# Kernel tuning notes

Hardware: AMD Instinct MI355X
Metric: run time of the kernel (lower is better)

## Reference

```python
import jax, jax.numpy as jnp
import numpy as np

N_NODES = 50000
N_EDGES = 800000
N_GRAPHS = 64
HID = 128
FEAT = 64
OUT = 32
N_LAYERS = 3
DECAY = 0.9
THRESH = 0.1


def setup_inputs() -> dict:
    key = jax.random.key(0)
    ks = jax.random.split(key, 24)
    s = 0.05
    inp = {
        "x": jax.random.normal(ks[0], (N_NODES, FEAT), jnp.float32),
        "edge_attr": jax.random.normal(ks[1], (N_EDGES, 1), jnp.float32),
        "initial_importance": jax.random.uniform(ks[2], (N_NODES, 1), jnp.float32),
        "imp_proj_W": jax.random.normal(ks[3], (1, HID), jnp.float32) * s,
        "imp_proj_b": jnp.zeros((HID,), jnp.float32),
        "init_W": jax.random.normal(ks[4], (FEAT + HID, HID), jnp.float32) * s,
        "init_b": jnp.zeros((HID,), jnp.float32),
        "msg_W": jax.random.normal(ks[5], (N_LAYERS, HID, HID), jnp.float32) * s,
        "msg_b": jnp.zeros((N_LAYERS, HID), jnp.float32),
        "upd_W": jax.random.normal(ks[6], (N_LAYERS, 2 * HID, HID), jnp.float32) * s,
        "upd_b": jnp.zeros((N_LAYERS, HID), jnp.float32),
        "gate_W": jax.random.normal(ks[7], (N_LAYERS, HID + 1, HID), jnp.float32) * s,
        "gate_b": jnp.zeros((N_LAYERS, HID), jnp.float32),
        "prop_W": jax.random.normal(ks[8], (N_LAYERS, HID, 1), jnp.float32) * s,
        "prop_b": jnp.zeros((N_LAYERS, 1), jnp.float32),
        "norm_w": jnp.ones((N_LAYERS, HID), jnp.float32),
        "norm_b": jnp.zeros((N_LAYERS, HID), jnp.float32),
        "norm_a": jnp.ones((N_LAYERS, HID), jnp.float32),
        "final_W": jax.random.normal(ks[9], (HID, OUT), jnp.float32) * s,
        "final_b": jnp.zeros((OUT,), jnp.float32),
        "edge_index": jax.random.randint(ks[10], (2, N_EDGES), 0, N_NODES, jnp.int32),
        # evenly spread sorted graph ids -> every graph non-empty
        "batch": (jnp.arange(N_NODES, dtype=jnp.int32) * N_GRAPHS) // N_NODES,
    }
    return inp


def _normalize_importance(imp, batch):
    # per-graph min/max normalization, fused segment reductions
    mn = jax.ops.segment_min(imp, batch, num_segments=N_GRAPHS)[batch]
    mx = jax.ops.segment_max(imp, batch, num_segments=N_GRAPHS)[batch]
    return (imp - mn) / (mx - mn + 1e-8)


def _graph_norm(x, batch, counts, w, b, a):
    # PyG GraphNorm: y = w * (x - a*mean) / sqrt(var(x - a*mean) + eps) + b
    mean = jax.ops.segment_sum(x, batch, num_segments=N_GRAPHS) / counts
    out = x - a * mean[batch]
    var = jax.ops.segment_sum(out * out, batch, num_segments=N_GRAPHS) / counts
    std = jnp.sqrt(var + 1e-5)
    return w * out / std[batch] + b


def _forward(x, edge_attr, initial_importance, imp_proj_W, imp_proj_b, init_W,
             init_b, msg_W, msg_b, upd_W, upd_b, gate_W, gate_b, prop_W, prop_b,
             norm_w, norm_b, norm_a, final_W, final_b, edge_index, batch):
    src, dst = edge_index[0], edge_index[1]
    counts = jax.ops.segment_sum(jnp.ones((N_NODES, 1), x.dtype), batch,
                                 num_segments=N_GRAPHS)  # [G,1]

    imp0 = initial_importance[:, 0]                       # [N]
    importance = _normalize_importance(imp0, batch)       # [N]
    imp_emb = importance[:, None] @ imp_proj_W + imp_proj_b  # [N,H]
    h = jnp.concatenate([x, imp_emb], axis=-1) @ init_W + init_b  # [N,H]

    for l in range(N_LAYERS):
        # MPNN: gather -> linear -> scatter-add -> update
        msg = h[src] @ msg_W[l] + msg_b[l]                # [E,H]
        aggr = jax.ops.segment_sum(msg, dst, num_segments=N_NODES)  # [N,H]
        conv = jnp.concatenate([h, aggr], axis=-1) @ upd_W[l] + upd_b[l]
        # importance gating
        gate_in = jnp.concatenate([conv, importance[:, None]], axis=-1)
        gate = jax.nn.sigmoid(gate_in @ gate_W[l] + gate_b[l])
        out = gate * conv + (1.0 - gate) * h
        prop = out @ prop_W[l] + prop_b[l]                # [N,1]
        # norm + relu (dropout p=0 in eval)
        h = jax.nn.relu(_graph_norm(out, batch, counts, norm_w[l], norm_b[l], norm_a[l]))
        # importance update
        imp = DECAY * importance + (1.0 - DECAY) * prop[:, 0]
        imp = _normalize_importance(imp, batch)
        imp = jnp.where(imp < THRESH, 0.0, imp)
        importance = _normalize_importance(imp, batch)

    h = h @ final_W + final_b                             # [N,OUT]
    logits = jax.ops.segment_sum(h, batch, num_segments=N_GRAPHS) / counts  # [G,OUT]
    final_importance = _normalize_importance(imp0 + importance, batch)
    return logits, final_importance[:, None]


def reference(x, edge_attr, initial_importance, imp_proj_W, imp_proj_b, init_W,
              init_b, msg_W, msg_b, upd_W, upd_b, gate_W, gate_b, prop_W, prop_b,
              norm_w, norm_b, norm_a, final_W, final_b, edge_index, batch):
    return _forward(x, edge_attr, initial_importance, imp_proj_W, imp_proj_b,
                    init_W, init_b, msg_W, msg_b, upd_W, upd_b, gate_W, gate_b,
                    prop_W, prop_b, norm_w, norm_b, norm_a, final_W, final_b,
                    edge_index, batch)
```

## Files before the change

### kernel.cpp

```cpp
#include <hip/hip_runtime.h>
#include <cstdint>

#define NN 50000
#define NE 800000
#define NG 64
#define HD 128
#define FT 64
#define NLAYERS 3
#define MB 32
#define NBLK 1563

__global__ void k_gbounds(const int* __restrict__ batch, int* __restrict__ gstart){
    int i = blockIdx.x*blockDim.x + threadIdx.x;
    if (i >= NN) return;
    int g = batch[i];
    if (i == 0){ for (int q = 0; q <= g; ++q) gstart[q] = 0; }
    else { int gp = batch[i-1]; for (int q = gp+1; q <= g; ++q) gstart[q] = i; }
    if (i == NN-1){ for (int q = g+1; q <= NG; ++q) gstart[q] = NN; }
}

__device__ __forceinline__ void block_minmax(float lmn, float lmx, float* red,
                                             float& omn, float& omx){
    #pragma unroll
    for (int off = 32; off > 0; off >>= 1){
        lmn = fminf(lmn, __shfl_xor(lmn, off));
        lmx = fmaxf(lmx, __shfl_xor(lmx, off));
    }
    int wave = threadIdx.x >> 6;
    if ((threadIdx.x & 63) == 0){ red[wave] = lmn; red[4+wave] = lmx; }
    __syncthreads();
    omn = fminf(fminf(red[0], red[1]), fminf(red[2], red[3]));
    omx = fmaxf(fmaxf(red[4], red[5]), fmaxf(red[6], red[7]));
    __syncthreads();
}

__global__ __launch_bounds__(256) void k_norm_graph(
    const float* __restrict__ va, const int* __restrict__ gstart,
    float* __restrict__ out)
{
    __shared__ float sv[1024];
    __shared__ float red[8];
    int g = blockIdx.x;
    int s = gstart[g], n = gstart[g+1] - s;
    int tid = threadIdx.x;
    float lmn = 3.4e38f, lmx = -3.4e38f;
    for (int i = tid; i < n; i += 256){
        float v = va[s+i];
        sv[i] = v;
        lmn = fminf(lmn, v); lmx = fmaxf(lmx, v);
    }
    float lo, hi;
    block_minmax(lmn, lmx, red, lo, hi);
    float inv = 1.f/(hi - lo + 1e-8f);
    for (int i = tid; i < n; i += 256) out[s+i] = (sv[i] - lo)*inv;
}

__global__ void k_fold_init(const float* __restrict__ pW, const float* __restrict__ pb,
                            const float* __restrict__ iW, const float* __restrict__ ib,
                            float* __restrict__ W0, float* __restrict__ b0){
    int j = threadIdx.x;
    for (int k = 0; k < FT; ++k) W0[k*HD + j] = iW[k*HD + j];
    float w2 = 0.f, b2 = 0.f;
    for (int k = 0; k < HD; ++k){
        float w = iW[(FT + k)*HD + j];
        w2 += pW[k]*w;
        b2 += pb[k]*w;
    }
    W0[FT*HD + j] = w2;
    b0[j] = ib[j] + b2;
}

__global__ void k_fold_layer(const float* __restrict__ msgW, const float* __restrict__ updW,
                             const float* __restrict__ msgb,
                             float* __restrict__ WfA, float* __restrict__ bcvA){
    int l = blockIdx.y;
    const float* mW  = msgW + (size_t)l*HD*HD;
    const float* uW  = updW + (size_t)l*2*HD*HD;
    const float* mb  = msgb + (size_t)l*HD;
    float* Wf  = WfA  + (size_t)l*2*HD*HD;
    float* bcv = bcvA + (size_t)l*HD;
    int j = threadIdx.x;
    int r = blockIdx.x;
    if (r < HD){
        Wf[(size_t)r*HD + j] = uW[(size_t)r*HD + j];
    } else if (r < 2*HD){
        int rr = r - HD;
        const float* uWbot = uW + (size_t)HD*HD;
        float acc = 0.f;
        for (int k = 0; k < HD; ++k)
            acc = fmaf(mW[(size_t)rr*HD + k], uWbot[(size_t)k*HD + j], acc);
        Wf[(size_t)r*HD + j] = acc;
    } else {
        const float* uWbot = uW + (size_t)HD*HD;
        float acc = 0.f;
        for (int k = 0; k < HD; ++k)
            acc = fmaf(mb[k], uWbot[(size_t)k*HD + j], acc);
        bcv[j] = acc;
    }
}

__global__ __launch_bounds__(256) void k_init(
    const float* __restrict__ x, const float* __restrict__ imp,
    const float* __restrict__ W0, const float* __restrict__ b0v,
    float* __restrict__ h)
{
    __shared__ float lds[MB][FT];
    __shared__ float scs[MB];
    int base = blockIdx.x*MB, tid = threadIdx.x;
    #pragma unroll
    for (int i = 0; i < 2; ++i){
        int fidx = i*256 + tid;
        int t = fidx >> 4, c = fidx & 15;
        float4 v = {0.f,0.f,0.f,0.f};
        if (base + t < NN) v = *(const float4*)&x[(size_t)(base+t)*FT + c*4];
        *(float4*)&lds[t][c*4] = v;
    }
    if (tid < MB) scs[tid] = (base+tid < NN) ? imp[base+tid] : 0.f;
    __syncthreads();

    const int cg = tid & 31, rg = tid >> 5;
    const int c0 = cg*4, r0 = rg*4;
    const float4 wl4 = *(const float4*)&W0[(size_t)FT*HD + c0];
    const float4 b4  = *(const float4*)&b0v[c0];
    float acc[4][4];
    #pragma unroll
    for (int r = 0; r < 4; ++r){
        float s = scs[r0+r];
        acc[r][0] = fmaf(s, wl4.x, b4.x); acc[r][1] = fmaf(s, wl4.y, b4.y);
        acc[r][2] = fmaf(s, wl4.z, b4.z); acc[r][3] = fmaf(s, wl4.w, b4.w);
    }
    #pragma unroll 4
    for (int k4 = 0; k4 < 16; ++k4){
        const float4 w0 = *(const float4*)&W0[(size_t)(k4*4+0)*HD + c0];
        const float4 w1 = *(const float4*)&W0[(size_t)(k4*4+1)*HD + c0];
        const float4 w2 = *(const float4*)&W0[(size_t)(k4*4+2)*HD + c0];
        const float4 w3 = *(const float4*)&W0[(size_t)(k4*4+3)*HD + c0];
        #pragma unroll
        for (int r = 0; r < 4; ++r){
            const float4 a = *(const float4*)&lds[r0+r][k4*4];
            acc[r][0]=fmaf(a.x,w0.x,fmaf(a.y,w1.x,fmaf(a.z,w2.x,fmaf(a.w,w3.x,acc[r][0]))));
            acc[r][1]=fmaf(a.x,w0.y,fmaf(a.y,w1.y,fmaf(a.z,w2.y,fmaf(a.w,w3.y,acc[r][1]))));
            acc[r][2]=fmaf(a.x,w0.z,fmaf(a.y,w1.z,fmaf(a.z,w2.z,fmaf(a.w,w3.z,acc[r][2]))));
            acc[r][3]=fmaf(a.x,w0.w,fmaf(a.y,w1.w,fmaf(a.z,w2.w,fmaf(a.w,w3.w,acc[r][3]))));
        }
    }
    #pragma unroll
    for (int r = 0; r < 4; ++r)
        if (base + r0 + r < NN)
            *(float4*)&h[(size_t)(base+r0+r)*HD + c0] =
                make_float4(acc[r][0], acc[r][1], acc[r][2], acc[r][3]);
}

#define FMA8(r, a, b, W0_,W1_,W2_,W3_,W4_,W5_,W6_,W7_, A) \
    A[r][0]=fmaf((b).x,W4_.x,fmaf((b).y,W5_.x,fmaf((b).z,W6_.x,fmaf((b).w,W7_.x, \
            fmaf((a).x,W0_.x,fmaf((a).y,W1_.x,fmaf((a).z,W2_.x,fmaf((a).w,W3_.x,A[r][0])))))))); \
    A[r][1]=fmaf((b).x,W4_.y,fmaf((b).y,W5_.y,fmaf((b).z,W6_.y,fmaf((b).w,W7_.y, \
            fmaf((a).x,W0_.y,fmaf((a).y,W1_.y,fmaf((a).z,W2_.y,fmaf((a).w,W3_.y,A[r][1])))))))); \
    A[r][2]=fmaf((b).x,W4_.z,fmaf((b).y,W5_.z,fmaf((b).z,W6_.z,fmaf((b).w,W7_.z, \
            fmaf((a).x,W0_.z,fmaf((a).y,W1_.z,fmaf((a).z,W2_.z,fmaf((a).w,W3_.z,A[r][2])))))))); \
    A[r][3]=fmaf((b).x,W4_.w,fmaf((b).y,W5_.w,fmaf((b).z,W6_.w,fmaf((b).w,W7_.w, \
            fmaf((a).x,W0_.w,fmaf((a).y,W1_.w,fmaf((a).z,W2_.w,fmaf((a).w,W3_.w,A[r][3]))))))));

__global__ __launch_bounds__(256, 4) void k_layer(
    const float* __restrict__ h, const float* __restrict__ aggr,
    const float* __restrict__ imp, const int* __restrict__ deg,
    const float* __restrict__ Wf, const float* __restrict__ bcv,
    const float* __restrict__ ub,
    const float* __restrict__ gW, const float* __restrict__ gb,
    const float* __restrict__ prW, const float* __restrict__ prb,
    float* __restrict__ outbuf, float* __restrict__ ta)
{
    __shared__ float lds[MB][256];
    __shared__ float scs[MB];
    __shared__ float dgs[MB];
    __shared__ float red[8][4];
    const int base = blockIdx.x*MB, tid = threadIdx.x;

    #pragma unroll
    for (int i = 0; i < 8; ++i){
        int fidx = i*256 + tid;
        int t = fidx >> 6, c = fidx & 63;
        float4 v = {0.f,0.f,0.f,0.f};
        if (base + t < NN){
            const float* srcp = (c < 32) ? &h[(size_t)(base+t)*HD + c*4]
                                         : &aggr[(size_t)(base+t)*HD + (c-32)*4];
            v = *(const float4*)srcp;
        }
        *(float4*)&lds[t][c*4] = v;
    }
    if (tid < MB) scs[tid] = (base+tid < NN) ? imp[base+tid] : 0.f;
    else if (tid < 2*MB){
        int t = tid - MB;
        dgs[t] = (base+t < NN) ? (float)deg[base+t] : 0.f;
    }
    __syncthreads();

    const int cg = tid & 31, rg = tid >> 5;
    const int c0 = cg*4, r0 = rg*4;

    const float4* wv = (const float4*)Wf;
    const float4 bc4 = *(const float4*)&bcv[c0];
    const float4 ub4 = *(const float4*)&ub[c0];
    float acc[4][4];
    #pragma unroll
    for (int r = 0; r < 4; ++r){
        float d = dgs[r0+r];
        acc[r][0] = fmaf(d, bc4.x, ub4.x); acc[r][1] = fmaf(d, bc4.y, ub4.y);
        acc[r][2] = fmaf(d, bc4.z, ub4.z); acc[r][3] = fmaf(d, bc4.w, ub4.w);
    }
    {
        const float4* p0 = wv + cg;
        float4 n0 = p0[0],   n1 = p0[32],  n2 = p0[64],  n3 = p0[96];
        float4 n4 = p0[128], n5 = p0[160], n6 = p0[192], n7 = p0[224];
        for (int kb = 0; kb < 256; kb += 8){
            const float4 w0=n0,w1=n1,w2=n2,w3=n3,w4=n4,w5=n5,w6=n6,w7=n7;
            if (kb + 8 < 256){
                const float4* np = wv + (size_t)(kb+8)*32 + cg;
                n0=np[0];   n1=np[32];  n2=np[64];  n3=np[96];
                n4=np[128]; n5=np[160]; n6=np[192]; n7=np[224];
            }
            #pragma unroll
            for (int r = 0; r < 4; ++r){
                const float4 a = *(const float4*)&lds[r0+r][kb];
                const float4 b = *(const float4*)&lds[r0+r][kb+4];
                FMA8(r, a, b, w0,w1,w2,w3,w4,w5,w6,w7, acc)
            }
        }
    }
    __syncthreads();
    #pragma unroll
    for (int r = 0; r < 4; ++r)
        *(float4*)&lds[r0+r][HD + c0] = make_float4(acc[r][0],acc[r][1],acc[r][2],acc[r][3]);
    __syncthreads();

    const float4* gv = (const float4*)gW;
    const float4 gwl = gv[(size_t)HD*32 + cg];
    const float4 gb4 = *(const float4*)&gb[c0];
    float z[4][4];
    #pragma unroll
    for (int r = 0; r < 4; ++r){
        float s = scs[r0+r];
        z[r][0] = fmaf(s, gwl.x, gb4.x); z[r][1] = fmaf(s, gwl.y, gb4.y);
        z[r][2] = fmaf(s, gwl.z, gb4.z); z[r][3] = fmaf(s, gwl.w, gb4.w);
    }
    {
        const float4* p0 = gv + cg;
        float4 n0 = p0[0],   n1 = p0[32],  n2 = p0[64],  n3 = p0[96];
        float4 n4 = p0[128], n5 = p0[160], n6 = p0[192], n7 = p0[224];
        for (int kb = 0; kb < 128; kb += 8){
            const float4 w0=n0,w1=n1,w2=n2,w3=n3,w4=n4,w5=n5,w6=n6,w7=n7;
            if (kb + 8 < 128){
                const float4* np = gv + (size_t)(kb+8)*32 + cg;
                n0=np[0];   n1=np[32];  n2=np[64];  n3=np[96];
                n4=np[128]; n5=np[160]; n6=np[192]; n7=np[224];
            }
            #pragma unroll
            for (int r = 0; r < 4; ++r){
                const float4 a = *(const float4*)&lds[r0+r][HD + kb];
                const float4 b = *(const float4*)&lds[r0+r][HD + kb+4];
                FMA8(r, a, b, w0,w1,w2,w3,w4,w5,w6,w7, z)
            }
        }
    }

    const float4 pr4 = *(const float4*)&prW[c0];
    float psum[4];
    #pragma unroll
    for (int r = 0; r < 4; ++r){
        const float4 hv = *(const float4*)&lds[r0+r][c0];
        float g0 = 1.f/(1.f + expf(-z[r][0]));
        float g1 = 1.f/(1.f + expf(-z[r][1]));
        float g2 = 1.f/(1.f + expf(-z[r][2]));
        float g3 = 1.f/(1.f + expf(-z[r][3]));
        float o0 = g0*acc[r][0] + (1.f-g0)*hv.x;
        float o1 = g1*acc[r][1] + (1.f-g1)*hv.y;
        float o2 = g2*acc[r][2] + (1.f-g2)*hv.z;
        float o3 = g3*acc[r][3] + (1.f-g3)*hv.w;
        if (base + r0 + r < NN)
            *(float4*)&outbuf[(size_t)(base+r0+r)*HD + c0] = make_float4(o0,o1,o2,o3);
        psum[r] = o0*pr4.x + o1*pr4.y + o2*pr4.z + o3*pr4.w;
    }
    #pragma unroll
    for (int r = 0; r < 4; ++r){
        float v = psum[r];
        #pragma unroll
        for (int off = 16; off > 0; off >>= 1) v += __shfl_xor(v, off);
        if (cg == 0) red[rg][r] = v;
    }
    __syncthreads();
    if (tid < MB && base + tid < NN)
        ta[base+tid] = 0.9f*scs[tid] + 0.1f*(red[tid>>2][tid&3] + prb[0]);
}

__global__ void k_deg(const int* __restrict__ dst, int* deg){
    int e = blockIdx.x*blockDim.x + threadIdx.x;
    if (e < NE) atomicAdd(&deg[dst[e]], 1);
}

__global__ __launch_bounds__(1024) void k_scan(const int* __restrict__ deg,
                                               int* __restrict__ rowstart){
    __shared__ int wtot[16];
    __shared__ int woff[16];
    __shared__ int carry;
    int tid = threadIdx.x, lane = tid & 63, wv = tid >> 6;
    if (tid == 0) carry = 0;
    __syncthreads();
    for (int base = 0; base < NN; base += 1024){
        int i = base + tid;
        int v = (i < NN) ? deg[i] : 0;
        int x = v;
        #pragma unroll
        for (int off = 1; off < 64; off <<= 1){
            int y = __shfl_up(x, off);
            if (lane >= off) x += y;
        }
        if (lane == 63) wtot[wv] = x;
        __syncthreads();
        if (tid == 0){
            int a = carry;
            for (int w2 = 0; w2 < 16; ++w2){ woff[w2] = a; a += wtot[w2]; }
            carry = a;
        }
        __syncthreads();
        if (i < NN) rowstart[i] = woff[wv] + x - v;
    }
    __syncthreads();
    if (tid == 0) rowstart[NN] = carry;
}

__global__ void k_copy_int(const int* __restrict__ a, int* __restrict__ b, int n){
    int i = blockIdx.x*blockDim.x + threadIdx.x;
    if (i < n) b[i] = a[i];
}

__global__ void k_fill(const int* __restrict__ src, const int* __restrict__ dst,
                       int* cursor, int* __restrict__ csr){
    int e = blockIdx.x*blockDim.x + threadIdx.x;
    if (e < NE){
        int d = dst[e];
        int p = atomicAdd(&cursor[d], 1);
        csr[p] = src[e];
    }
}

__global__ __launch_bounds__(256) void k_aggregate(
    const float* __restrict__ hm, const int* __restrict__ rowstart,
    const int* __restrict__ csr, float* __restrict__ aggr)
{
    int node = blockIdx.x*8 + (threadIdx.x >> 5);
    int lane = threadIdx.x & 31;
    float4 a0 = {0.f,0.f,0.f,0.f}, a1 = a0, a2 = a0, a3 = a0;
    float4 a4 = a0, a5 = a0, a6 = a0, a7 = a0;
    int e0 = rowstart[node], e1 = rowstart[node+1];
    int e = e0;
    for (; e + 7 < e1; e += 8){
        int s0 = csr[e],   s1 = csr[e+1], s2 = csr[e+2], s3 = csr[e+3];
        int s4 = csr[e+4], s5 = csr[e+5], s6 = csr[e+6], s7 = csr[e+7];
        const float4 v0 = *(const float4*)&hm[(size_t)s0*HD + lane*4];
        const float4 v1 = *(const float4*)&hm[(size_t)s1*HD + lane*4];
        const float4 v2 = *(const float4*)&hm[(size_t)s2*HD + lane*4];
        const float4 v3 = *(const float4*)&hm[(size_t)s3*HD + lane*4];
        const float4 v4 = *(const float4*)&hm[(size_t)s4*HD + lane*4];
        const float4 v5 = *(const float4*)&hm[(size_t)s5*HD + lane*4];
        const float4 v6 = *(const float4*)&hm[(size_t)s6*HD + lane*4];
        const float4 v7 = *(const float4*)&hm[(size_t)s7*HD + lane*4];
        a0.x += v0.x; a0.y += v0.y; a0.z += v0.z; a0.w += v0.w;
        a1.x += v1.x; a1.y += v1.y; a1.z += v1.z; a1.w += v1.w;
        a2.x += v2.x; a2.y += v2.y; a2.z += v2.z; a2.w += v2.w;
        a3.x += v3.x; a3.y += v3.y; a3.z += v3.z; a3.w += v3.w;
        a4.x += v4.x; a4.y += v4.y; a4.z += v4.z; a4.w += v4.w;
        a5.x += v5.x; a5.y += v5.y; a5.z += v5.z; a5.w += v5.w;
        a6.x += v6.x; a6.y += v6.y; a6.z += v6.z; a6.w += v6.w;
        a7.x += v7.x; a7.y += v7.y; a7.z += v7.z; a7.w += v7.w;
    }
    for (; e + 3 < e1; e += 4){
        int s0 = csr[e], s1 = csr[e+1], s2 = csr[e+2], s3 = csr[e+3];
        const float4 v0 = *(const float4*)&hm[(size_t)s0*HD + lane*4];
        const float4 v1 = *(const float4*)&hm[(size_t)s1*HD + lane*4];
        const float4 v2 = *(const float4*)&hm[(size_t)s2*HD + lane*4];
        const float4 v3 = *(const float4*)&hm[(size_t)s3*HD + lane*4];
        a0.x += v0.x; a0.y += v0.y; a0.z += v0.z; a0.w += v0.w;
        a1.x += v1.x; a1.y += v1.y; a1.z += v1.z; a1.w += v1.w;
        a2.x += v2.x; a2.y += v2.y; a2.z += v2.z; a2.w += v2.w;
        a3.x += v3.x; a3.y += v3.y; a3.z += v3.z; a3.w += v3.w;
    }
    for (; e < e1; ++e){
        int s0 = csr[e];
        const float4 v0 = *(const float4*)&hm[(size_t)s0*HD + lane*4];
        a0.x += v0.x; a0.y += v0.y; a0.z += v0.z; a0.w += v0.w;
    }
    a0.x += a1.x; a0.y += a1.y; a0.z += a1.z; a0.w += a1.w;
    a2.x += a3.x; a2.y += a3.y; a2.z += a3.z; a2.w += a3.w;
    a4.x += a5.x; a4.y += a5.y; a4.z += a5.z; a4.w += a5.w;
    a6.x += a7.x; a6.y += a7.y; a6.z += a7.z; a6.w += a7.w;
    a0.x += a2.x; a0.y += a2.y; a0.z += a2.z; a0.w += a2.w;
    a4.x += a6.x; a4.y += a6.y; a4.z += a6.z; a4.w += a6.w;
    a0.x += a4.x; a0.y += a4.y; a0.z += a4.z; a0.w += a4.w;
    *(float4*)&aggr[(size_t)node*HD + lane*4] = a0;
}

__global__ __launch_bounds__(256) void k_gnorm(
    const float* __restrict__ v, const int* __restrict__ gstart,
    const float* __restrict__ nw, const float* __restrict__ nb,
    const float* __restrict__ na, float* __restrict__ hout,
    const float* __restrict__ tsrc, float* __restrict__ tdst)
{
    int g = blockIdx.x;
    int part = blockIdx.y;
    int s = gstart[g], n = gstart[g+1] - s;
    int tid = threadIdx.x;

    if (part == 4){
        __shared__ float sv[1024];
        __shared__ float red[8];
        float lmn = 3.4e38f, lmx = -3.4e38f;
        for (int i = tid; i < n; i += 256){
            float val = tsrc[s+i]; sv[i] = val;
            lmn = fminf(lmn, val); lmx = fmaxf(lmx, val);
        }
        float lo, hi;
        block_minmax(lmn, lmx, red, lo, hi);
        float inv = 1.f/(hi - lo + 1e-8f);
        lmn = 3.4e38f; lmx = -3.4e38f;
        for (int i = tid; i < n; i += 256){
            float t2 = (sv[i] - lo)*inv;
            if (t2 < 0.1f) t2 = 0.f;
            sv[i] = t2;
            lmn = fminf(lmn, t2); lmx = fmaxf(lmx, t2);
        }
        float lo2, hi2;
        block_minmax(lmn, lmx, red, lo2, hi2);
        float inv2 = 1.f/(hi2 - lo2 + 1e-8f);
        for (int i = tid; i < n; i += 256) tdst[s+i] = (sv[i] - lo2)*inv2;
        return;
    }

    __shared__ float4 rs1[32][8];
    __shared__ float4 rs2[32][8];
    __shared__ float amv[32], scv[32], nbv[32];
    int rg = tid >> 3, c4l = tid & 7;
    size_t coff = (size_t)part*32 + c4l*4;
    float4 s1 = {0.f,0.f,0.f,0.f}, s2 = {0.f,0.f,0.f,0.f};
    for (int i = rg; i < n; i += 32){
        const float4 vv = *(const float4*)&v[(size_t)(s+i)*HD + coff];
        s1.x += vv.x; s1.y += vv.y; s1.z += vv.z; s1.w += vv.w;
        s2.x += vv.x*vv.x; s2.y += vv.y*vv.y; s2.z += vv.z*vv.z; s2.w += vv.w*vv.w;
    }
    rs1[rg][c4l] = s1; rs2[rg][c4l] = s2;
    __syncthreads();
    if (tid < 8){
        float4 t1 = {0.f,0.f,0.f,0.f}, t2 = {0.f,0.f,0.f,0.f};
        for (int r = 0; r < 32; ++r){
            float4 a = rs1[r][tid]; float4 b = rs2[r][tid];
            t1.x += a.x; t1.y += a.y; t1.z += a.z; t1.w += a.w;
            t2.x += b.x; t2.y += b.y; t2.z += b.z; t2.w += b.w;
        }
        float fn = (float)n;
        float S1[4] = {t1.x,t1.y,t1.z,t1.w};
        float S2[4] = {t2.x,t2.y,t2.z,t2.w};
        #pragma unroll
        for (int e = 0; e < 4; ++e){
            int j = part*32 + tid*4 + e;
            float m = S1[e]/fn;
            float aj = na[j];
            float var = S2[e]/fn - (2.f*aj - aj*aj)*m*m;
            float stdv = sqrtf(var + 1e-5f);
            amv[tid*4+e] = aj*m;
            scv[tid*4+e] = nw[j]/stdv;
            nbv[tid*4+e] = nb[j];
        }
    }
    __syncthreads();
    const float4 am4 = *(const float4*)&amv[c4l*4];
    const float4 sc4 = *(const float4*)&scv[c4l*4];
    const float4 nb4 = *(const float4*)&nbv[c4l*4];
    for (int i = rg; i < n; i += 32){
        const float4 vv = *(const float4*)&v[(size_t)(s+i)*HD + coff];
        float4 r;
        r.x = fmaxf((vv.x - am4.x)*sc4.x + nb4.x, 0.f);
        r.y = fmaxf((vv.y - am4.y)*sc4.y + nb4.y, 0.f);
        r.z = fmaxf((vv.z - am4.z)*sc4.z + nb4.z, 0.f);
        r.w = fmaxf((vv.w - am4.w)*sc4.w + nb4.w, 0.f);
        *(float4*)&hout[(size_t)(s+i)*HD + coff] = r;
    }
}

__global__ __launch_bounds__(1024) void k_logits(
    const float* __restrict__ h, const int* __restrict__ gstart,
    const float* __restrict__ fW, const float* __restrict__ fb,
    const float* __restrict__ imp0, const float* __restrict__ impf,
    float* __restrict__ outp)
{
    __shared__ float4 rs1[32][32];
    __shared__ float gsum[HD];
    __shared__ float redn[32];
    int g = blockIdx.x;
    int s = gstart[g], n = gstart[g+1] - s;
    int tid = threadIdx.x;
    int c4 = tid & 31, rg = tid >> 5;
    float4 s1 = {0.f,0.f,0.f,0.f};
    for (int i = rg; i < n; i += 32){
        const float4 vv = *(const float4*)&h[(size_t)(s+i)*HD + c4*4];
        s1.x += vv.x; s1.y += vv.y; s1.z += vv.z; s1.w += vv.w;
    }
    rs1[rg][c4] = s1;
    __syncthreads();
    if (tid < 32){
        float4 t1 = {0.f,0.f,0.f,0.f};
        for (int r = 0; r < 32; ++r){
            float4 a = rs1[r][tid];
            t1.x += a.x; t1.y += a.y; t1.z += a.z; t1.w += a.w;
        }
        gsum[tid*4+0] = t1.x; gsum[tid*4+1] = t1.y;
        gsum[tid*4+2] = t1.z; gsum[tid*4+3] = t1.w;
    }
    __syncthreads();
    if (tid < 32){
        int o = tid;
        float acc = 0.f;
        for (int k = 0; k < HD; ++k) acc = fmaf(gsum[k], fW[k*32 + o], acc);
        outp[g*32 + o] = acc/(float)n + fb[o];
    }
    float val = 0.f;
    bool has = (tid < n);
    float lmn = 3.4e38f, lmx = -3.4e38f;
    if (has){ val = imp0[s+tid] + impf[s+tid]; lmn = val; lmx = val; }
    #pragma unroll
    for (int off = 32; off > 0; off >>= 1){
        lmn = fminf(lmn, __shfl_xor(lmn, off));
        lmx = fmaxf(lmx, __shfl_xor(lmx, off));
    }
    int wv = tid >> 6, lane = tid & 63;
    if (lane == 0){ redn[wv] = lmn; redn[16+wv] = lmx; }
    __syncthreads();
    float lo = redn[0], hi = redn[16];
    for (int r2 = 1; r2 < 16; ++r2){
        lo = fminf(lo, redn[r2]); hi = fmaxf(hi, redn[16+r2]);
    }
    if (has) outp[NG*32 + s + tid] = (val - lo)/(hi - lo + 1e-8f);
}

extern "C" void kernel_launch(void* const* d_in, const int* in_sizes, int n_in,
                              void* d_out, int out_size, void* d_ws, size_t ws_size,
                              hipStream_t stream){
    const float* x    = (const float*)d_in[0];
    const float* imp0 = (const float*)d_in[2];
    const float* pW   = (const float*)d_in[3];
    const float* pb   = (const float*)d_in[4];
    const float* iW   = (const float*)d_in[5];
    const float* ib   = (const float*)d_in[6];
    const float* msgW = (const float*)d_in[7];
    const float* msgb = (const float*)d_in[8];
    const float* updW = (const float*)d_in[9];
    const float* updb = (const float*)d_in[10];
    const float* gWt  = (const float*)d_in[11];
    const float* gb   = (const float*)d_in[12];
    const float* prW  = (const float*)d_in[13];
    const float* prb  = (const float*)d_in[14];
    const float* nw   = (const float*)d_in[15];
    const float* nb   = (const float*)d_in[16];
    const float* na   = (const float*)d_in[17];
    const float* fW   = (const float*)d_in[18];
    const float* fb   = (const float*)d_in[19];
    const int* eidx   = (const int*)d_in[20];
    const int* batch  = (const int*)d_in[21];
    const int* esrc = eidx;
    const int* edst = eidx + NE;
    float* outp = (float*)d_out;

    char* w = (char*)d_ws;
    size_t off = 0;
    auto alloc = [&](size_t bytes)->char*{
        char* p = w + off;
        off += (bytes + 255) & ~(size_t)255;
        return p;
    };
    float* h     = (float*)alloc((size_t)NN*HD*4);
    float* aggB  = (float*)alloc((size_t)NN*HD*4);
    float* outA  = (float*)alloc((size_t)NN*HD*4);
    float* ta    = (float*)alloc((size_t)NN*4);
    float* imp   = (float*)alloc((size_t)NN*4);
    float* W0    = (float*)alloc((size_t)(FT+1)*HD*4);
    float* b0    = (float*)alloc((size_t)HD*4);
    float* Wf    = (float*)alloc((size_t)NLAYERS*2*HD*HD*4);
    float* bcv   = (float*)alloc((size_t)NLAYERS*HD*4);
    int* gstart  = (int*)alloc((size_t)(NG+1)*4);
    int* deg     = (int*)alloc((size_t)NN*4);
    int* rowst   = (int*)alloc((size_t)(NN+1)*4);
    int* cursor  = (int*)alloc((size_t)NN*4);
    int* csr     = (int*)alloc((size_t)NE*4);

    k_gbounds<<<196, 256, 0, stream>>>(batch, gstart);

    hipMemsetAsync(deg, 0, NN*4, stream);
    k_deg<<<3125, 256, 0, stream>>>(edst, deg);
    k_scan<<<1, 1024, 0, stream>>>(deg, rowst);
    k_copy_int<<<196, 256, 0, stream>>>(rowst, cursor, NN);
    k_fill<<<3125, 256, 0, stream>>>(esrc, edst, cursor, csr);

    k_fold_init<<<1, 128, 0, stream>>>(pW, pb, iW, ib, W0, b0);
    k_fold_layer<<<dim3(257, NLAYERS), 128, 0, stream>>>(msgW, updW, msgb, Wf, bcv);

    k_norm_graph<<<NG, 256, 0, stream>>>(imp0, gstart, imp);
    k_init<<<NBLK, 256, 0, stream>>>(x, imp, W0, b0, h);

    for (int l = 0; l < NLAYERS; ++l){
        k_aggregate<<<6250, 256, 0, stream>>>(h, rowst, csr, aggB);
        k_layer<<<NBLK, 256, 0, stream>>>(
            h, aggB, imp, deg,
            Wf + (size_t)l*2*HD*HD, bcv + (size_t)l*HD,
            updb + (size_t)l*HD, gWt + (size_t)l*(HD+1)*HD, gb + (size_t)l*HD,
            prW + (size_t)l*HD, prb + l, outA, ta);
        k_gnorm<<<dim3(NG,5), 256, 0, stream>>>(outA, gstart,
            nw + (size_t)l*HD, nb + (size_t)l*HD, na + (size_t)l*HD, h, ta, imp);
    }

    k_logits<<<NG, 1024, 0, stream>>>(h, gstart, fW, fb, imp0, imp, outp);
}
```

Measured before the change: 738.4 us.

## Stage layer weight tiles through LDS with register double-buffering

The per-layer fused GEMM kernel no longer streams weight float4s straight from global memory into each thread. It now loads 32-row weight tiles cooperatively into a shared-memory buffer and prefetches the next tile into registers while computing on the current one, for both the update and gate matmuls. This is meant to cut redundant global/L2 weight traffic, since each of the eight row-groups previously fetched the same weights. In exchange it adds 16 KB of LDS per block, two barriers per tile, and lowers the launch-bounds occupancy hint from 4 to 3 blocks.

```diff
diff --git a/kernel.cpp b/kernel.cpp
--- a/kernel.cpp
+++ b/kernel.cpp
@@ -161,7 +161,7 @@
     A[r][3]=fmaf((b).x,W4_.w,fmaf((b).y,W5_.w,fmaf((b).z,W6_.w,fmaf((b).w,W7_.w, \
             fmaf((a).x,W0_.w,fmaf((a).y,W1_.w,fmaf((a).z,W2_.w,fmaf((a).w,W3_.w,A[r][3]))))))));
 
-__global__ __launch_bounds__(256, 4) void k_layer(
+__global__ __launch_bounds__(256, 3) void k_layer(
     const float* __restrict__ h, const float* __restrict__ aggr,
     const float* __restrict__ imp, const int* __restrict__ deg,
     const float* __restrict__ Wf, const float* __restrict__ bcv,
@@ -171,10 +171,12 @@
     float* __restrict__ outbuf, float* __restrict__ ta)
 {
     __shared__ float lds[MB][256];
+    __shared__ float wlds[32][HD];
     __shared__ float scs[MB];
     __shared__ float dgs[MB];
     __shared__ float red[8][4];
     const int base = blockIdx.x*MB, tid = threadIdx.x;
+    float4* wl4 = (float4*)wlds;
 
     #pragma unroll
     for (int i = 0; i < 8; ++i){
@@ -193,12 +195,14 @@
         int t = tid - MB;
         dgs[t] = (base+t < NN) ? (float)deg[base+t] : 0.f;
     }
-    __syncthreads();
 
     const int cg = tid & 31, rg = tid >> 5;
     const int c0 = cg*4, r0 = rg*4;
 
-    const float4* wv = (const float4*)Wf;
+    const float4* wv4 = (const float4*)Wf;
+    float4 wr0 = wv4[tid], wr1 = wv4[256+tid], wr2 = wv4[512+tid], wr3 = wv4[768+tid];
+    __syncthreads();
+
     const float4 bc4 = *(const float4*)&bcv[c0];
     const float4 ub4 = *(const float4*)&ub[c0];
     float acc[4][4];
@@ -208,33 +212,42 @@
         acc[r][0] = fmaf(d, bc4.x, ub4.x); acc[r][1] = fmaf(d, bc4.y, ub4.y);
         acc[r][2] = fmaf(d, bc4.z, ub4.z); acc[r][3] = fmaf(d, bc4.w, ub4.w);
     }
-    {
-        const float4* p0 = wv + cg;
-        float4 n0 = p0[0],   n1 = p0[32],  n2 = p0[64],  n3 = p0[96];
-        float4 n4 = p0[128], n5 = p0[160], n6 = p0[192], n7 = p0[224];
-        for (int kb = 0; kb < 256; kb += 8){
-            const float4 w0=n0,w1=n1,w2=n2,w3=n3,w4=n4,w5=n5,w6=n6,w7=n7;
-            if (kb + 8 < 256){
-                const float4* np = wv + (size_t)(kb+8)*32 + cg;
-                n0=np[0];   n1=np[32];  n2=np[64];  n3=np[96];
-                n4=np[128]; n5=np[160]; n6=np[192]; n7=np[224];
-            }
+    for (int t = 0; t < 8; ++t){
+        __syncthreads();
+        wl4[tid] = wr0; wl4[256+tid] = wr1; wl4[512+tid] = wr2; wl4[768+tid] = wr3;
+        __syncthreads();
+        if (t < 7){
+            const float4* np = wv4 + (size_t)(t+1)*1024;
+            wr0 = np[tid]; wr1 = np[256+tid]; wr2 = np[512+tid]; wr3 = np[768+tid];
+        }
+        const int kb0 = t*32;
+        #pragma unroll
+        for (int kk = 0; kk < 32; kk += 8){
+            const float4 w0 = *(const float4*)&wlds[kk+0][c0];
+            const float4 w1 = *(const float4*)&wlds[kk+1][c0];
+            const float4 w2 = *(const float4*)&wlds[kk+2][c0];
+            const float4 w3 = *(const float4*)&wlds[kk+3][c0];
+            const float4 w4 = *(const float4*)&wlds[kk+4][c0];
+            const float4 w5 = *(const float4*)&wlds[kk+5][c0];
+            const float4 w6 = *(const float4*)&wlds[kk+6][c0];
+            const float4 w7 = *(const float4*)&wlds[kk+7][c0];
             #pragma unroll
             for (int r = 0; r < 4; ++r){
-                const float4 a = *(const float4*)&lds[r0+r][kb];
-                const float4 b = *(const float4*)&lds[r0+r][kb+4];
+                const float4 a = *(const float4*)&lds[r0+r][kb0+kk];
+                const float4 b = *(const float4*)&lds[r0+r][kb0+kk+4];
                 FMA8(r, a, b, w0,w1,w2,w3,w4,w5,w6,w7, acc)
             }
         }
     }
     __syncthreads();
+
     #pragma unroll
     for (int r = 0; r < 4; ++r)
         *(float4*)&lds[r0+r][HD + c0] = make_float4(acc[r][0],acc[r][1],acc[r][2],acc[r][3]);
-    __syncthreads();
-
-    const float4* gv = (const float4*)gW;
-    const float4 gwl = gv[(size_t)HD*32 + cg];
+    const float4* gv4 = (const float4*)gW;
+    wr0 = gv4[tid]; wr1 = gv4[256+tid]; wr2 = gv4[512+tid]; wr3 = gv4[768+tid];
+
+    const float4 gwl = gv4[(size_t)HD*32 + cg];
     const float4 gb4 = *(const float4*)&gb[c0];
     float z[4][4];
     #pragma unroll
@@ -243,21 +256,29 @@
         z[r][0] = fmaf(s, gwl.x, gb4.x); z[r][1] = fmaf(s, gwl.y, gb4.y);
         z[r][2] = fmaf(s, gwl.z, gb4.z); z[r][3] = fmaf(s, gwl.w, gb4.w);
     }
-    {
-        const float4* p0 = gv + cg;
-        float4 n0 = p0[0],   n1 = p0[32],  n2 = p0[64],  n3 = p0[96];
-        float4 n4 = p0[128], n5 = p0[160], n6 = p0[192], n7 = p0[224];
-        for (int kb = 0; kb < 128; kb += 8){
-            const float4 w0=n0,w1=n1,w2=n2,w3=n3,w4=n4,w5=n5,w6=n6,w7=n7;
-            if (kb + 8 < 128){
-                const float4* np = gv + (size_t)(kb+8)*32 + cg;
-                n0=np[0];   n1=np[32];  n2=np[64];  n3=np[96];
-                n4=np[128]; n5=np[160]; n6=np[192]; n7=np[224];
-            }
+    for (int t = 0; t < 4; ++t){
+        __syncthreads();
+        wl4[tid] = wr0; wl4[256+tid] = wr1; wl4[512+tid] = wr2; wl4[768+tid] = wr3;
+        __syncthreads();
+        if (t < 3){
+            const float4* np = gv4 + (size_t)(t+1)*1024;
+            wr0 = np[tid]; wr1 = np[256+tid]; wr2 = np[512+tid]; wr3 = np[768+tid];
+        }
+        const int kb0 = t*32;
+        #pragma unroll
+        for (int kk = 0; kk < 32; kk += 8){
+            const float4 w0 = *(const float4*)&wlds[kk+0][c0];
+            const float4 w1 = *(const float4*)&wlds[kk+1][c0];
+            const float4 w2 = *(const float4*)&wlds[kk+2][c0];
+            const float4 w3 = *(const float4*)&wlds[kk+3][c0];
+            const float4 w4 = *(const float4*)&wlds[kk+4][c0];
+            const float4 w5 = *(const float4*)&wlds[kk+5][c0];
+            const float4 w6 = *(const float4*)&wlds[kk+6][c0];
+            const float4 w7 = *(const float4*)&wlds[kk+7][c0];
             #pragma unroll
             for (int r = 0; r < 4; ++r){
-                const float4 a = *(const float4*)&lds[r0+r][HD + kb];
-                const float4 b = *(const float4*)&lds[r0+r][HD + kb+4];
+                const float4 a = *(const float4*)&lds[r0+r][HD + kb0+kk];
+                const float4 b = *(const float4*)&lds[r0+r][HD + kb0+kk+4];
                 FMA8(r, a, b, w0,w1,w2,w3,w4,w5,w6,w7, z)
             }
         }
```

Result: slower. 890.1 us (+20.5%).

## Stage layer weights and activations into LDS via async DMA double buffering

Applied to the files above, without the earlier changes.

The fused layer kernel now copies its h/aggr tiles and 32-row weight slices straight from global memory into LDS with global_load_lds. The weight slices are double-buffered, so the next slice loads while the current one is consumed. Previously every thread fetched weights from global/L2 into registers, so each wave re-read the full matrices. In exchange the kernel uses about 64 KB of LDS and adds a barrier per K-slice, and launch bounds drop to 2 blocks per CU. The unguarded DMA of the last partial row tile may read past the end of the arrays.

```diff
diff --git a/kernel.cpp b/kernel.cpp
--- a/kernel.cpp
+++ b/kernel.cpp
@@ -9,6 +9,12 @@
 #define NLAYERS 3
 #define MB 32
 #define NBLK 1563
+
+__device__ __forceinline__ void dma16(const float* g, float* l){
+    __builtin_amdgcn_global_load_lds(
+        (const __attribute__((address_space(1))) void*)g,
+        (__attribute__((address_space(3))) void*)l, 16, 0, 0);
+}
 
 __global__ void k_gbounds(const int* __restrict__ batch, int* __restrict__ gstart){
     int i = blockIdx.x*blockDim.x + threadIdx.x;
@@ -161,7 +167,7 @@
     A[r][3]=fmaf((b).x,W4_.w,fmaf((b).y,W5_.w,fmaf((b).z,W6_.w,fmaf((b).w,W7_.w, \
             fmaf((a).x,W0_.w,fmaf((a).y,W1_.w,fmaf((a).z,W2_.w,fmaf((a).w,W3_.w,A[r][3]))))))));
 
-__global__ __launch_bounds__(256, 4) void k_layer(
+__global__ __launch_bounds__(256, 2) void k_layer(
     const float* __restrict__ h, const float* __restrict__ aggr,
     const float* __restrict__ imp, const int* __restrict__ deg,
     const float* __restrict__ Wf, const float* __restrict__ bcv,
@@ -170,37 +176,42 @@
     const float* __restrict__ prW, const float* __restrict__ prb,
     float* __restrict__ outbuf, float* __restrict__ ta)
 {
-    __shared__ float lds[MB][256];
+    __shared__ float hl[MB][HD];
+    __shared__ float al[MB][HD];
+    __shared__ float wbuf[2][32][HD];
     __shared__ float scs[MB];
     __shared__ float dgs[MB];
     __shared__ float red[8][4];
     const int base = blockIdx.x*MB, tid = threadIdx.x;
 
-    #pragma unroll
-    for (int i = 0; i < 8; ++i){
-        int fidx = i*256 + tid;
-        int t = fidx >> 6, c = fidx & 63;
-        float4 v = {0.f,0.f,0.f,0.f};
-        if (base + t < NN){
-            const float* srcp = (c < 32) ? &h[(size_t)(base+t)*HD + c*4]
-                                         : &aggr[(size_t)(base+t)*HD + (c-32)*4];
-            v = *(const float4*)srcp;
-        }
-        *(float4*)&lds[t][c*4] = v;
-    }
+    {
+        const float* hsrc = h    + (size_t)base*HD;
+        const float* asrc = aggr + (size_t)base*HD;
+        #pragma unroll
+        for (int i = 0; i < 4; ++i){
+            dma16(hsrc + i*1024 + tid*4, &hl[0][0] + i*1024 + tid*4);
+            dma16(asrc + i*1024 + tid*4, &al[0][0] + i*1024 + tid*4);
+        }
+    }
+    #pragma unroll
+    for (int i = 0; i < 4; ++i)
+        dma16(Wf + i*1024 + tid*4, &wbuf[0][0][0] + i*1024 + tid*4);
     if (tid < MB) scs[tid] = (base+tid < NN) ? imp[base+tid] : 0.f;
     else if (tid < 2*MB){
         int t = tid - MB;
         dgs[t] = (base+t < NN) ? (float)deg[base+t] : 0.f;
     }
-    __syncthreads();
 
     const int cg = tid & 31, rg = tid >> 5;
     const int c0 = cg*4, r0 = rg*4;
-
-    const float4* wv = (const float4*)Wf;
     const float4 bc4 = *(const float4*)&bcv[c0];
     const float4 ub4 = *(const float4*)&ub[c0];
+    const float4 gwl = *(const float4*)&gW[(size_t)HD*HD + c0];
+    const float4 gb4 = *(const float4*)&gb[c0];
+    const float4 pr4 = *(const float4*)&prW[c0];
+
+    __syncthreads();
+
     float acc[4][4];
     #pragma unroll
     for (int r = 0; r < 4; ++r){
@@ -208,34 +219,48 @@
         acc[r][0] = fmaf(d, bc4.x, ub4.x); acc[r][1] = fmaf(d, bc4.y, ub4.y);
         acc[r][2] = fmaf(d, bc4.z, ub4.z); acc[r][3] = fmaf(d, bc4.w, ub4.w);
     }
-    {
-        const float4* p0 = wv + cg;
-        float4 n0 = p0[0],   n1 = p0[32],  n2 = p0[64],  n3 = p0[96];
-        float4 n4 = p0[128], n5 = p0[160], n6 = p0[192], n7 = p0[224];
-        for (int kb = 0; kb < 256; kb += 8){
-            const float4 w0=n0,w1=n1,w2=n2,w3=n3,w4=n4,w5=n5,w6=n6,w7=n7;
-            if (kb + 8 < 256){
-                const float4* np = wv + (size_t)(kb+8)*32 + cg;
-                n0=np[0];   n1=np[32];  n2=np[64];  n3=np[96];
-                n4=np[128]; n5=np[160]; n6=np[192]; n7=np[224];
-            }
+    for (int t = 0; t < 8; ++t){
+        {
+            const float* nsrc = (t < 7) ? (Wf + (size_t)(t+1)*32*HD) : gW;
+            float* ndst = &wbuf[(t+1)&1][0][0];
+            #pragma unroll
+            for (int i = 0; i < 4; ++i)
+                dma16(nsrc + i*1024 + tid*4, ndst + i*1024 + tid*4);
+        }
+        const float (*A)[HD] = (t < 4) ? hl : al;
+        const int kb = (t & 3)*32;
+        const float (*W)[HD] = wbuf[t & 1];
+        #pragma unroll
+        for (int kk = 0; kk < 32; kk += 8){
+            const float4 w0 = *(const float4*)&W[kk+0][c0];
+            const float4 w1 = *(const float4*)&W[kk+1][c0];
+            const float4 w2 = *(const float4*)&W[kk+2][c0];
+            const float4 w3 = *(const float4*)&W[kk+3][c0];
+            const float4 w4 = *(const float4*)&W[kk+4][c0];
+            const float4 w5 = *(const float4*)&W[kk+5][c0];
+            const float4 w6 = *(const float4*)&W[kk+6][c0];
+            const float4 w7 = *(const float4*)&W[kk+7][c0];
             #pragma unroll
             for (int r = 0; r < 4; ++r){
-                const float4 a = *(const float4*)&lds[r0+r][kb];
-                const float4 b = *(const float4*)&lds[r0+r][kb+4];
+                const float4 a = *(const float4*)&A[r0+r][kb+kk];
+                const float4 b = *(const float4*)&A[r0+r][kb+kk+4];
                 FMA8(r, a, b, w0,w1,w2,w3,w4,w5,w6,w7, acc)
             }
         }
-    }
-    __syncthreads();
+        __syncthreads();
+    }
+
     #pragma unroll
     for (int r = 0; r < 4; ++r)
-        *(float4*)&lds[r0+r][HD + c0] = make_float4(acc[r][0],acc[r][1],acc[r][2],acc[r][3]);
-    __syncthreads();
-
-    const float4* gv = (const float4*)gW;
-    const float4 gwl = gv[(size_t)HD*32 + cg];
-    const float4 gb4 = *(const float4*)&gb[c0];
+        *(float4*)&al[r0+r][c0] = make_float4(acc[r][0],acc[r][1],acc[r][2],acc[r][3]);
+    {
+        const float* nsrc = gW + (size_t)32*HD;
+        #pragma unroll
+        for (int i = 0; i < 4; ++i)
+            dma16(nsrc + i*1024 + tid*4, &wbuf[1][0][0] + i*1024 + tid*4);
+    }
+    __syncthreads();
+
     float z[4][4];
     #pragma unroll
     for (int r = 0; r < 4; ++r){
@@ -243,31 +268,45 @@
         z[r][0] = fmaf(s, gwl.x, gb4.x); z[r][1] = fmaf(s, gwl.y, gb4.y);
         z[r][2] = fmaf(s, gwl.z, gb4.z); z[r][3] = fmaf(s, gwl.w, gb4.w);
     }
-    {
-        const float4* p0 = gv + cg;
-        float4 n0 = p0[0],   n1 = p0[32],  n2 = p0[64],  n3 = p0[96];
-        float4 n4 = p0[128], n5 = p0[160], n6 = p0[192], n7 = p0[224];
-        for (int kb = 0; kb < 128; kb += 8){
-            const float4 w0=n0,w1=n1,w2=n2,w3=n3,w4=n4,w5=n5,w6=n6,w7=n7;
-            if (kb + 8 < 128){
-                const float4* np = gv + (size_t)(kb+8)*32 + cg;
-                n0=np[0];   n1=np[32];  n2=np[64];  n3=np[96];
-                n4=np[128]; n5=np[160]; n6=np[192]; n7=np[224];
-            }
+    for (int t = 0; t < 4; ++t){
+        if (t < 2){
+            const float* nsrc = gW + (size_t)(t+2)*32*HD;
+            float* ndst = &wbuf[t&1][0][0];
+            (void)nsrc; (void)ndst;
+        }
+        const float (*W)[HD] = wbuf[t & 1];
+        const int kb = t*32;
+        #pragma unroll
+        for (int kk = 0; kk < 32; kk += 8){
+            const float4 w0 = *(const float4*)&W[kk+0][c0];
+            const float4 w1 = *(const float4*)&W[kk+1][c0];
+            const float4 w2 = *(const float4*)&W[kk+2][c0];
+            const float4 w3 = *(const float4*)&W[kk+3][c0];
+            const float4 w4 = *(const float4*)&W[kk+4][c0];
+            const float4 w5 = *(const float4*)&W[kk+5][c0];
+            const float4 w6 = *(const float4*)&W[kk+6][c0];
+            const float4 w7 = *(const float4*)&W[kk+7][c0];
             #pragma unroll
             for (int r = 0; r < 4; ++r){
-                const float4 a = *(const float4*)&lds[r0+r][HD + kb];
-                const float4 b = *(const float4*)&lds[r0+r][HD + kb+4];
+                const float4 a = *(const float4*)&al[r0+r][kb+kk];
+                const float4 b = *(const float4*)&al[r0+r][kb+kk+4];
                 FMA8(r, a, b, w0,w1,w2,w3,w4,w5,w6,w7, z)
             }
         }
-    }
-
-    const float4 pr4 = *(const float4*)&prW[c0];
+        __syncthreads();
+        if (t < 2){
+            const float* nsrc = gW + (size_t)(t+2)*32*HD;
+            float* ndst = &wbuf[t&1][0][0];
+            #pragma unroll
+            for (int i = 0; i < 4; ++i)
+                dma16(nsrc + i*1024 + tid*4, ndst + i*1024 + tid*4);
+        }
+    }
+
     float psum[4];
     #pragma unroll
     for (int r = 0; r < 4; ++r){
-        const float4 hv = *(const float4*)&lds[r0+r][c0];
+        const float4 hv = *(const float4*)&hl[r0+r][c0];
         float g0 = 1.f/(1.f + expf(-z[r][0]));
         float g1 = 1.f/(1.f + expf(-z[r][1]));
         float g2 = 1.f/(1.f + expf(-z[r][2]));
```

Result: slower. 777.8 us (+5.3%).
